# Optimization experiments

Measured on AMD Instinct MI355X. Metric: run time of the kernel, lower is better.

## Reference

```python
import jax, jax.numpy as jnp
import numpy as np

EPS = 1e-5

def layernorm(x, gamma, beta):
    # torch.var default is unbiased (ddof=1) - faithful to source
    m = jnp.mean(x, axis=-1, keepdims=True)
    d = x.shape[-1]
    var = jnp.sum((x - m) ** 2, axis=-1, keepdims=True) / (d - 1)
    return gamma * (x - m) / jnp.sqrt(var + EPS) + beta

def setup_inputs() -> dict:
    key = jax.random.key(0)
    B, S, D, H = 8, 1024, 768, 12
    hd = D // H
    ks = jax.random.split(key, 20)
    s_in = 1.0 / np.sqrt(D)
    s_ff = 1.0 / np.sqrt(4 * D)
    return {
        "x":  jax.random.normal(ks[0], (B, S, D), jnp.float32),
        "Wq": jax.random.uniform(ks[1], (H, D, hd), jnp.float32, -s_in, s_in),
        "bq": jax.random.uniform(ks[2], (H, hd), jnp.float32, -s_in, s_in),
        "Wk": jax.random.uniform(ks[3], (H, D, hd), jnp.float32, -s_in, s_in),
        "bk": jax.random.uniform(ks[4], (H, hd), jnp.float32, -s_in, s_in),
        "Wv": jax.random.uniform(ks[5], (H, D, hd), jnp.float32, -s_in, s_in),
        "bv": jax.random.uniform(ks[6], (H, hd), jnp.float32, -s_in, s_in),
        "Wo": jax.random.uniform(ks[7], (D, D), jnp.float32, -s_in, s_in),
        "bo": jax.random.uniform(ks[8], (D,), jnp.float32, -s_in, s_in),
        "W1": jax.random.uniform(ks[9], (D, 4 * D), jnp.float32, -s_in, s_in),
        "b1": jax.random.uniform(ks[10], (4 * D,), jnp.float32, -s_in, s_in),
        "W2": jax.random.uniform(ks[11], (4 * D, D), jnp.float32, -s_ff, s_ff),
        "b2": jax.random.uniform(ks[12], (D,), jnp.float32, -s_ff, s_ff),
        "g1": jnp.ones((D,), jnp.float32),
        "be1": jnp.zeros((D,), jnp.float32),
        "g2": jnp.ones((D,), jnp.float32),
        "be2": jnp.zeros((D,), jnp.float32),
    }

def reference(x, Wq, bq, Wk, bk, Wv, bv, Wo, bo, W1, b1, W2, b2, g1, be1, g2, be2):
    # x = ln1(x); x = x + mha(x); x = ln2(x); out = x + ffwd(x)
    x = layernorm(x, g1, be1)
    hd = Wq.shape[-1]
    q = jnp.einsum('bsd,hdk->bhsk', x, Wq) + bq[None, :, None, :]
    k = jnp.einsum('bsd,hdk->bhsk', x, Wk) + bk[None, :, None, :]
    v = jnp.einsum('bsd,hdk->bhsk', x, Wv) + bv[None, :, None, :]
    att = jnp.einsum('bhqk,bhsk->bhqs', q, k) * (hd ** -0.5)
    att = jax.nn.softmax(att, axis=-1)
    o = jnp.einsum('bhqs,bhsk->bhqk', att, v)  # [B,H,S,hd]
    B, H, S, _ = o.shape
    o = jnp.transpose(o, (0, 2, 1, 3)).reshape(B, S, H * hd)  # concat heads
    x = x + o @ Wo + bo
    x = layernorm(x, g2, be2)
    h = jax.nn.gelu(x @ W1 + b1, approximate=False)
    out = x + h @ W2 + b2
    return out
```

## Files before the change

### kernel.cpp

```cpp
#include <hip/hip_runtime.h>
#include <stdint.h>

typedef __attribute__((ext_vector_type(8))) short bf16x8;
typedef __attribute__((ext_vector_type(4))) float f32x4;

#define GPTR(p) ((const __attribute__((address_space(1))) void*)(p))
#define LPTR(p) ((__attribute__((address_space(3))) void*)(p))

__device__ __forceinline__ float b2f(unsigned short u) {
  union { unsigned int i; float f; } v; v.i = ((unsigned int)u) << 16; return v.f;
}
__device__ __forceinline__ unsigned short f2b(float f) {
  union { float f; unsigned int i; } v; v.f = f;
  unsigned int i = v.i;
  return (unsigned short)((i + 0x7FFFu + ((i >> 16) & 1u)) >> 16);
}

__global__ __launch_bounds__(256) void ln_kernel(const unsigned short* __restrict__ xin,
                                                 const float* __restrict__ g,
                                                 const float* __restrict__ be,
                                                 unsigned short* __restrict__ y) {
  const int D = 768;
  int row = blockIdx.x;
  int t = threadIdx.x;
  float v[3];
  float s = 0.f, s2 = 0.f;
#pragma unroll
  for (int i = 0; i < 3; ++i) {
    int c = t + i * 256;
    float f = b2f(xin[(size_t)row * D + c]);
    v[i] = f; s += f; s2 += f * f;
  }
#pragma unroll
  for (int d = 32; d > 0; d >>= 1) { s += __shfl_down(s, d); s2 += __shfl_down(s2, d); }
  __shared__ float red[8];
  int w = t >> 6;
  if ((t & 63) == 0) { red[w] = s; red[4 + w] = s2; }
  __syncthreads();
  s = red[0] + red[1] + red[2] + red[3];
  s2 = red[4] + red[5] + red[6] + red[7];
  float mean = s * (1.0f / 768.0f);
  float var = (s2 - 768.0f * mean * mean) * (1.0f / 767.0f);
  float rstd = rsqrtf(var + 1e-5f);
  unsigned short* yr = y + (size_t)row * D;
#pragma unroll
  for (int i = 0; i < 3; ++i) {
    int c = t + i * 256;
    yr[c] = f2b((v[i] - mean) * rstd * g[c] + be[c]);
  }
}

__global__ __launch_bounds__(256) void prep_kernel(const float* __restrict__ Wq,
                                                   const float* __restrict__ Wk,
                                                   const float* __restrict__ Wv,
                                                   const float* __restrict__ Wo,
                                                   const float* __restrict__ W1,
                                                   const float* __restrict__ W2,
                                                   const float* __restrict__ x,
                                                   const float* __restrict__ g1,
                                                   const float* __restrict__ be1,
                                                   unsigned short* __restrict__ Wqkvt,
                                                   unsigned short* __restrict__ Wot,
                                                   unsigned short* __restrict__ W1t,
                                                   unsigned short* __restrict__ W2t,
                                                   unsigned short* __restrict__ y) {
  int bid = blockIdx.x;
  int t = threadIdx.x;
  if (bid < 6912) {
    __shared__ float tile[32][33];
    const float* in; unsigned short* out; int R, C, c0, r0;
    if (bid < 1728) {
      int seg = bid / 576, r = bid % 576;
      int z = r / 48, t2 = r % 48, bx = t2 & 1, by = t2 >> 1;
      in = (seg == 0 ? Wq : seg == 1 ? Wk : Wv) + (size_t)z * 768 * 64;
      out = Wqkvt + (size_t)seg * 768 * 768 + (size_t)z * 64 * 768;
      R = 768; C = 64; c0 = bx * 32; r0 = by * 32;
    } else if (bid < 2304) {
      int r = bid - 1728, bx = r % 24, by = r / 24;
      in = Wo; out = Wot; R = 768; C = 768; c0 = bx * 32; r0 = by * 32;
    } else if (bid < 4608) {
      int r = bid - 2304, bx = r % 96, by = r / 96;
      in = W1; out = W1t; R = 768; C = 3072; c0 = bx * 32; r0 = by * 32;
    } else {
      int r = bid - 4608, bx = r % 24, by = r / 24;
      in = W2; out = W2t; R = 3072; C = 768; c0 = bx * 32; r0 = by * 32;
    }
    int tc = t & 31, tr = t >> 5;
#pragma unroll
    for (int i = 0; i < 4; ++i) {
      int r = tr + i * 8;
      tile[r][tc] = in[(size_t)(r0 + r) * C + c0 + tc];
    }
    __syncthreads();
#pragma unroll
    for (int i = 0; i < 4; ++i) {
      int r = tr + i * 8;
      out[(size_t)(c0 + r) * R + r0 + tc] = f2b(tile[tc][r]);
    }
  } else {
    const int D = 768;
    int row = bid - 6912;
    float v[3];
    float s = 0.f, s2 = 0.f;
#pragma unroll
    for (int i = 0; i < 3; ++i) {
      int c = t + i * 256;
      float f = x[(size_t)row * D + c];
      v[i] = f; s += f; s2 += f * f;
    }
#pragma unroll
    for (int d = 32; d > 0; d >>= 1) { s += __shfl_down(s, d); s2 += __shfl_down(s2, d); }
    __shared__ float red[8];
    int w = t >> 6;
    if ((t & 63) == 0) { red[w] = s; red[4 + w] = s2; }
    __syncthreads();
    s = red[0] + red[1] + red[2] + red[3];
    s2 = red[4] + red[5] + red[6] + red[7];
    float mean = s * (1.0f / 768.0f);
    float var = (s2 - 768.0f * mean * mean) * (1.0f / 767.0f);
    float rstd = rsqrtf(var + 1e-5f);
    unsigned short* yr = y + (size_t)row * D;
#pragma unroll
    for (int i = 0; i < 3; ++i) {
      int c = t + i * 256;
      yr[c] = f2b((v[i] - mean) * rstd * g1[c] + be1[c]);
    }
  }
}

template <int EPI>
__global__ __launch_bounds__(256) void gemm_bt(const unsigned short* __restrict__ A,
                                               const unsigned short* __restrict__ Bt,
                                               int M, int N, int K,
                                               const float* __restrict__ bias0,
                                               const float* __restrict__ bias1,
                                               const float* __restrict__ bias2,
                                               const unsigned short* __restrict__ res,
                                               unsigned short* __restrict__ out0,
                                               unsigned short* __restrict__ out1,
                                               unsigned short* __restrict__ out2,
                                               float* __restrict__ outf) {
  __shared__ unsigned short As[2][128 * 32];
  __shared__ unsigned short Bs[2][128 * 32];
  int t = threadIdx.x;
  int n0 = blockIdx.x * 128, m0 = blockIdx.y * 128;
  int lane = t & 63, w = t >> 6;
  int lr = lane & 15, quad = lane >> 4;
  int wm = (w >> 1) * 64, wn = (w & 1) * 64;
  int rowInWave = lane >> 2;
  int colq = (lane & 3) * 8;
  f32x4 zero4 = {0.f, 0.f, 0.f, 0.f};
  f32x4 acc[4][4];
#pragma unroll
  for (int i = 0; i < 4; ++i)
#pragma unroll
    for (int j = 0; j < 4; ++j) acc[i][j] = zero4;
  for (int k0 = 0; k0 < K; k0 += 64) {
    __syncthreads();
#pragma unroll
    for (int s = 0; s < 2; ++s) {
#pragma unroll
      for (int rnd = 0; rnd < 2; ++rnd) {
        int rbase = rnd * 64 + w * 16;
        int row = rbase + rowInWave;
        __builtin_amdgcn_global_load_lds(GPTR(A + (size_t)(m0 + row) * K + k0 + s * 32 + colq),
                                         LPTR(&As[s][rbase * 32]), 16, 0, 0);
        __builtin_amdgcn_global_load_lds(GPTR(Bt + (size_t)(n0 + row) * K + k0 + s * 32 + colq),
                                         LPTR(&Bs[s][rbase * 32]), 16, 0, 0);
      }
    }
    __syncthreads();
#pragma unroll
    for (int s = 0; s < 2; ++s) {
      bf16x8 af[4];
#pragma unroll
      for (int i = 0; i < 4; ++i)
        af[i] = *(const bf16x8*)(&As[s][(wm + i * 16 + lr) * 32 + quad * 8]);
#pragma unroll
      for (int j = 0; j < 4; ++j) {
        bf16x8 bfr = *(const bf16x8*)(&Bs[s][(wn + j * 16 + lr) * 32 + quad * 8]);
#pragma unroll
        for (int i = 0; i < 4; ++i)
          acc[i][j] = __builtin_amdgcn_mfma_f32_16x16x32_bf16(af[i], bfr, acc[i][j], 0, 0, 0);
      }
    }
  }
#pragma unroll
  for (int i = 0; i < 4; ++i) {
#pragma unroll
    for (int j = 0; j < 4; ++j) {
#pragma unroll
      for (int r = 0; r < 4; ++r) {
        int rg = m0 + wm + i * 16 + quad * 4 + r;
        int cg = n0 + wn + j * 16 + lr;
        float val = acc[i][j][r];
        if (EPI == 1) {
          int b = rg >> 10, sx = rg & 1023;
          if (cg < 768) {
            int h = cg >> 6, kk = cg & 63;
            out0[(((size_t)(b * 12 + h) << 10) + sx) * 64 + kk] = f2b(val + bias0[cg]);
          } else if (cg < 1536) {
            int cc = cg - 768, h = cc >> 6, kk = cc & 63;
            out1[(((size_t)(b * 12 + h) << 10) + sx) * 64 + kk] = f2b(val + bias1[cc]);
          } else {
            int cc = cg - 1536, h = cc >> 6, kk = cc & 63;
            out2[((size_t)(b * 12 + h) << 16) + ((size_t)kk << 10) + sx] = f2b(val + bias2[cc]);
          }
        } else if (EPI == 2) {
          val += bias0[cg] + b2f(res[(size_t)rg * N + cg]);
          out0[(size_t)rg * N + cg] = f2b(val);
        } else if (EPI == 3) {
          float xg = val + bias0[cg];
          val = 0.5f * xg * (1.0f + erff(xg * 0.70710678118654752f));
          out0[(size_t)rg * N + cg] = f2b(val);
        } else if (EPI == 4) {
          outf[(size_t)rg * N + cg] = val + bias0[cg] + b2f(res[(size_t)rg * N + cg]);
        }
      }
    }
  }
}

__global__ __launch_bounds__(256) void attn_kernel(const unsigned short* __restrict__ q,
                                                   const unsigned short* __restrict__ k,
                                                   const unsigned short* __restrict__ vt,
                                                   unsigned short* __restrict__ out) {
  __shared__ unsigned short Ks[64 * 72];
  __shared__ unsigned short Vs[64 * 72];
  __shared__ unsigned short Ps[4][32 * 72];
  int bh = blockIdx.y;
  int q0 = blockIdx.x * 128;
  int t = threadIdx.x, lane = t & 63, w = t >> 6;
  int lr = lane & 15, quad = lane >> 4;
  const unsigned short* qb = q + (size_t)bh * 1024 * 64;
  const unsigned short* kb = k + (size_t)bh * 1024 * 64;
  const unsigned short* vb = vt + (size_t)bh * 64 * 1024;
  bf16x8 aq[2][2];
#pragma unroll
  for (int i = 0; i < 2; ++i)
#pragma unroll
    for (int ks = 0; ks < 2; ++ks)
      aq[i][ks] = *(const bf16x8*)(qb + (size_t)(q0 + w * 32 + i * 16 + lr) * 64 + ks * 32 + quad * 8);
  f32x4 zero4 = {0.f, 0.f, 0.f, 0.f};
  f32x4 oacc[2][4];
  float l_part[2][4];
#pragma unroll
  for (int i = 0; i < 2; ++i)
#pragma unroll
    for (int j = 0; j < 4; ++j) oacc[i][j] = zero4;
#pragma unroll
  for (int i = 0; i < 2; ++i)
#pragma unroll
    for (int r = 0; r < 4; ++r) l_part[i][r] = 0.f;
  int srow = t >> 3, spart = t & 7;
  unsigned short* ps = &Ps[w][0];
  for (int st = 0; st < 16; ++st) {
    int s0 = st * 64;
    __syncthreads();
#pragma unroll
    for (int rnd = 0; rnd < 2; ++rnd) {
      int rr = rnd * 32 + srow;
      *(uint4*)(&Ks[rr * 72 + spart * 8]) = *(const uint4*)(kb + (size_t)(s0 + rr) * 64 + spart * 8);
      *(uint4*)(&Vs[rr * 72 + spart * 8]) = *(const uint4*)(vb + (size_t)rr * 1024 + s0 + spart * 8);
    }
    __syncthreads();
#pragma unroll
    for (int i = 0; i < 2; ++i) {
#pragma unroll
      for (int j = 0; j < 4; ++j) {
        bf16x8 bk0 = *(const bf16x8*)(&Ks[(j * 16 + lr) * 72 + quad * 8]);
        bf16x8 bk1 = *(const bf16x8*)(&Ks[(j * 16 + lr) * 72 + 32 + quad * 8]);
        f32x4 z = zero4;
        z = __builtin_amdgcn_mfma_f32_16x16x32_bf16(aq[i][0], bk0, z, 0, 0, 0);
        z = __builtin_amdgcn_mfma_f32_16x16x32_bf16(aq[i][1], bk1, z, 0, 0, 0);
#pragma unroll
        for (int r = 0; r < 4; ++r) {
          float p = __expf(z[r] * 0.125f);
          l_part[i][r] += p;
          ps[(i * 16 + quad * 4 + r) * 72 + j * 16 + lr] = f2b(p);
        }
      }
    }
    __syncthreads();
#pragma unroll
    for (int i = 0; i < 2; ++i) {
#pragma unroll
      for (int ks = 0; ks < 2; ++ks) {
        bf16x8 ap = *(const bf16x8*)(&ps[(i * 16 + lr) * 72 + ks * 32 + quad * 8]);
#pragma unroll
        for (int j = 0; j < 4; ++j) {
          bf16x8 bv = *(const bf16x8*)(&Vs[(j * 16 + lr) * 72 + ks * 32 + quad * 8]);
          oacc[i][j] = __builtin_amdgcn_mfma_f32_16x16x32_bf16(ap, bv, oacc[i][j], 0, 0, 0);
        }
      }
    }
  }
  int b = bh / 12, h = bh % 12;
#pragma unroll
  for (int i = 0; i < 2; ++i) {
#pragma unroll
    for (int r = 0; r < 4; ++r) {
      float l = l_part[i][r];
#pragma unroll
      for (int d = 1; d < 16; d <<= 1) l += __shfl_xor(l, d);
      float inv = 1.0f / l;
      int sx = q0 + w * 32 + i * 16 + quad * 4 + r;
      size_t base = ((size_t)(b * 1024 + sx)) * 768 + h * 64;
#pragma unroll
      for (int j = 0; j < 4; ++j)
        out[base + j * 16 + lr] = f2b(oacc[i][j][r] * inv);
    }
  }
}

extern "C" void kernel_launch(void* const* d_in, const int* in_sizes, int n_in,
                              void* d_out, int out_size, void* d_ws, size_t ws_size,
                              hipStream_t stream) {
  const float* x  = (const float*)d_in[0];
  const float* Wq = (const float*)d_in[1];
  const float* bq = (const float*)d_in[2];
  const float* Wk = (const float*)d_in[3];
  const float* bk = (const float*)d_in[4];
  const float* Wv = (const float*)d_in[5];
  const float* bv = (const float*)d_in[6];
  const float* Wo = (const float*)d_in[7];
  const float* bo = (const float*)d_in[8];
  const float* W1 = (const float*)d_in[9];
  const float* b1 = (const float*)d_in[10];
  const float* W2 = (const float*)d_in[11];
  const float* b2 = (const float*)d_in[12];
  const float* g1 = (const float*)d_in[13];
  const float* be1= (const float*)d_in[14];
  const float* g2 = (const float*)d_in[15];
  const float* be2= (const float*)d_in[16];
  float* outf = (float*)d_out;

  const size_t SLOT = (size_t)8192 * 768;
  unsigned short* ws = (unsigned short*)d_ws;
  unsigned short* Wqkvt = ws;
  unsigned short* Wot   = Wqkvt + (size_t)2304 * 768;
  unsigned short* W1t   = Wot   + (size_t)768 * 768;
  unsigned short* W2t   = W1t   + (size_t)3072 * 768;
  unsigned short* s0    = W2t   + (size_t)768 * 3072;
  unsigned short* s1    = s0 + SLOT;
  unsigned short* s2    = s1 + SLOT;
  unsigned short* s3    = s2 + SLOT;
  unsigned short* s4    = s3 + SLOT;

  unsigned short* qbuf = s0;
  unsigned short* kbuf = s1;
  unsigned short* y    = s2;
  unsigned short* x2   = s3;
  unsigned short* ao   = s4;
  unsigned short* y2   = s4;
  unsigned short* hb   = s0;
  unsigned short* vtb  = (unsigned short*)d_out;

  prep_kernel<<<6912 + 8192, 256, 0, stream>>>(Wq, Wk, Wv, Wo, W1, W2, x, g1, be1,
                                               Wqkvt, Wot, W1t, W2t, y);

  gemm_bt<1><<<dim3(18, 64), 256, 0, stream>>>(y, Wqkvt, 8192, 2304, 768,
                                               bq, bk, bv, nullptr, qbuf, kbuf, vtb, nullptr);
  attn_kernel<<<dim3(8, 96), 256, 0, stream>>>(qbuf, kbuf, vtb, ao);
  gemm_bt<2><<<dim3(6, 64), 256, 0, stream>>>(ao, Wot, 8192, 768, 768,
                                              bo, nullptr, nullptr, y, x2, nullptr, nullptr, nullptr);
  ln_kernel<<<8192, 256, 0, stream>>>(x2, g2, be2, y2);
  gemm_bt<3><<<dim3(24, 64), 256, 0, stream>>>(y2, W1t, 8192, 3072, 768,
                                               b1, nullptr, nullptr, nullptr, hb, nullptr, nullptr, nullptr);
  gemm_bt<4><<<dim3(6, 64), 256, 0, stream>>>(hb, W2t, 8192, 768, 3072,
                                              b2, nullptr, nullptr, y2, nullptr, nullptr, nullptr, outf);
}
```

Before: 443.6 us.

## Give each wave private double-buffered LDS tiles and drop block barriers

The GEMM main loop is restructured so that each wave loads its own 64-row strips of A and B into a private, double-buffered LDS region with global_load_lds. The next K-slice is prefetched while the current one is consumed, and explicit vmcnt waits replace the two __syncthreads per iteration. The aim is to remove block-wide barrier stalls and overlap loads with MFMA work. In exchange, waves that share the same rows now load them separately, so global/L2 traffic rises, LDS use grows to 64KB per block (which may lower occupancy), and the K step shrinks to 32.

```diff
diff --git a/kernel.cpp b/kernel.cpp
--- a/kernel.cpp
+++ b/kernel.cpp
@@ -140,51 +140,58 @@
                                                unsigned short* __restrict__ out1,
                                                unsigned short* __restrict__ out2,
                                                float* __restrict__ outf) {
-  __shared__ unsigned short As[2][128 * 32];
-  __shared__ unsigned short Bs[2][128 * 32];
+  __shared__ unsigned short L[4][2][2][64 * 32];
   int t = threadIdx.x;
   int n0 = blockIdx.x * 128, m0 = blockIdx.y * 128;
   int lane = t & 63, w = t >> 6;
   int lr = lane & 15, quad = lane >> 4;
   int wm = (w >> 1) * 64, wn = (w & 1) * 64;
-  int rowInWave = lane >> 2;
-  int colq = (lane & 3) * 8;
+  int drow = lane >> 2;
+  int dcol = (lane & 3) * 8;
+  const unsigned short* Ab = A + (size_t)(m0 + wm) * K;
+  const unsigned short* Bb = Bt + (size_t)(n0 + wn) * K;
   f32x4 zero4 = {0.f, 0.f, 0.f, 0.f};
   f32x4 acc[4][4];
 #pragma unroll
   for (int i = 0; i < 4; ++i)
 #pragma unroll
     for (int j = 0; j < 4; ++j) acc[i][j] = zero4;
-  for (int k0 = 0; k0 < K; k0 += 64) {
-    __syncthreads();
-#pragma unroll
-    for (int s = 0; s < 2; ++s) {
-#pragma unroll
-      for (int rnd = 0; rnd < 2; ++rnd) {
-        int rbase = rnd * 64 + w * 16;
-        int row = rbase + rowInWave;
-        __builtin_amdgcn_global_load_lds(GPTR(A + (size_t)(m0 + row) * K + k0 + s * 32 + colq),
-                                         LPTR(&As[s][rbase * 32]), 16, 0, 0);
-        __builtin_amdgcn_global_load_lds(GPTR(Bt + (size_t)(n0 + row) * K + k0 + s * 32 + colq),
-                                         LPTR(&Bs[s][rbase * 32]), 16, 0, 0);
-      }
-    }
-    __syncthreads();
-#pragma unroll
-    for (int s = 0; s < 2; ++s) {
-      bf16x8 af[4];
+
+  const int niter = K >> 5;
+#pragma unroll
+  for (int g = 0; g < 4; ++g) {
+    __builtin_amdgcn_global_load_lds(GPTR(Ab + (size_t)(g * 16 + drow) * K + dcol),
+                                     LPTR(&L[w][0][0][g * 512]), 16, 0, 0);
+    __builtin_amdgcn_global_load_lds(GPTR(Bb + (size_t)(g * 16 + drow) * K + dcol),
+                                     LPTR(&L[w][0][1][g * 512]), 16, 0, 0);
+  }
+  for (int it = 0; it < niter; ++it) {
+    int cur = it & 1, nxt = cur ^ 1;
+    int kn = (it + 1 < niter ? it + 1 : it) << 5;
+#pragma unroll
+    for (int g = 0; g < 4; ++g) {
+      __builtin_amdgcn_global_load_lds(GPTR(Ab + (size_t)(g * 16 + drow) * K + kn + dcol),
+                                       LPTR(&L[w][nxt][0][g * 512]), 16, 0, 0);
+      __builtin_amdgcn_global_load_lds(GPTR(Bb + (size_t)(g * 16 + drow) * K + kn + dcol),
+                                       LPTR(&L[w][nxt][1][g * 512]), 16, 0, 0);
+    }
+    asm volatile("s_waitcnt vmcnt(8)" ::: "memory");
+    const unsigned short* as_ = &L[w][cur][0][0];
+    const unsigned short* bs_ = &L[w][cur][1][0];
+    bf16x8 af[4], bfr[4];
+#pragma unroll
+    for (int i = 0; i < 4; ++i)
+      af[i] = *(const bf16x8*)(&as_[(i * 16 + lr) * 32 + quad * 8]);
+#pragma unroll
+    for (int j = 0; j < 4; ++j)
+      bfr[j] = *(const bf16x8*)(&bs_[(j * 16 + lr) * 32 + quad * 8]);
+#pragma unroll
+    for (int j = 0; j < 4; ++j)
 #pragma unroll
       for (int i = 0; i < 4; ++i)
-        af[i] = *(const bf16x8*)(&As[s][(wm + i * 16 + lr) * 32 + quad * 8]);
-#pragma unroll
-      for (int j = 0; j < 4; ++j) {
-        bf16x8 bfr = *(const bf16x8*)(&Bs[s][(wn + j * 16 + lr) * 32 + quad * 8]);
-#pragma unroll
-        for (int i = 0; i < 4; ++i)
-          acc[i][j] = __builtin_amdgcn_mfma_f32_16x16x32_bf16(af[i], bfr, acc[i][j], 0, 0, 0);
-      }
-    }
-  }
+        acc[i][j] = __builtin_amdgcn_mfma_f32_16x16x32_bf16(af[i], bfr[j], acc[i][j], 0, 0, 0);
+  }
+  asm volatile("s_waitcnt vmcnt(0)" ::: "memory");
 #pragma unroll
   for (int i = 0; i < 4; ++i) {
 #pragma unroll
```

Result: slower. 497.4 us (+12.1%).

## Load GEMM A fragments directly from global and double-buffer B in LDS

Applied to the files above, without the earlier changes.

The GEMM no longer stages the A tile in shared memory: each wave reads its A MFMA fragments straight from global memory into registers. B is still staged in LDS, now double-buffered, with the next 32-wide K slice prefetched while the current one is consumed. This leaves one barrier per 32-wide K step instead of two per 64-wide step and halves the LDS footprint. In exchange, A global-load latency is exposed with no prefetch, the two waves that share the same rows load the same A data twice, and barriers happen more often.

```diff
diff --git a/kernel.cpp b/kernel.cpp
--- a/kernel.cpp
+++ b/kernel.cpp
@@ -140,7 +140,6 @@
                                                unsigned short* __restrict__ out1,
                                                unsigned short* __restrict__ out2,
                                                float* __restrict__ outf) {
-  __shared__ unsigned short As[2][128 * 32];
   __shared__ unsigned short Bs[2][128 * 32];
   int t = threadIdx.x;
   int n0 = blockIdx.x * 128, m0 = blockIdx.y * 128;
@@ -155,35 +154,44 @@
   for (int i = 0; i < 4; ++i)
 #pragma unroll
     for (int j = 0; j < 4; ++j) acc[i][j] = zero4;
-  for (int k0 = 0; k0 < K; k0 += 64) {
-    __syncthreads();
-#pragma unroll
-    for (int s = 0; s < 2; ++s) {
-#pragma unroll
-      for (int rnd = 0; rnd < 2; ++rnd) {
-        int rbase = rnd * 64 + w * 16;
-        int row = rbase + rowInWave;
-        __builtin_amdgcn_global_load_lds(GPTR(A + (size_t)(m0 + row) * K + k0 + s * 32 + colq),
-                                         LPTR(&As[s][rbase * 32]), 16, 0, 0);
-        __builtin_amdgcn_global_load_lds(GPTR(Bt + (size_t)(n0 + row) * K + k0 + s * 32 + colq),
-                                         LPTR(&Bs[s][rbase * 32]), 16, 0, 0);
-      }
-    }
-    __syncthreads();
-#pragma unroll
-    for (int s = 0; s < 2; ++s) {
-      bf16x8 af[4];
+
+  const unsigned short* arow[4];
+#pragma unroll
+  for (int i = 0; i < 4; ++i)
+    arow[i] = A + (size_t)(m0 + wm + i * 16 + lr) * K + quad * 8;
+
+  const int niter = K >> 5;
+#pragma unroll
+  for (int rnd = 0; rnd < 2; ++rnd) {
+    int rbase = rnd * 64 + w * 16;
+    __builtin_amdgcn_global_load_lds(GPTR(Bt + (size_t)(n0 + rbase + rowInWave) * K + colq),
+                                     LPTR(&Bs[0][rbase * 32]), 16, 0, 0);
+  }
+  for (int it = 0; it < niter; ++it) {
+    __syncthreads();
+    int cur = it & 1, nxt = cur ^ 1;
+    int k0 = it << 5;
+    int kn = (it + 1 < niter ? it + 1 : it) << 5;
+#pragma unroll
+    for (int rnd = 0; rnd < 2; ++rnd) {
+      int rbase = rnd * 64 + w * 16;
+      __builtin_amdgcn_global_load_lds(GPTR(Bt + (size_t)(n0 + rbase + rowInWave) * K + kn + colq),
+                                       LPTR(&Bs[nxt][rbase * 32]), 16, 0, 0);
+    }
+    bf16x8 af[4];
+#pragma unroll
+    for (int i = 0; i < 4; ++i)
+      af[i] = *(const bf16x8*)(arow[i] + k0);
+    const unsigned short* bs_ = &Bs[cur][0];
+    bf16x8 bfr[4];
+#pragma unroll
+    for (int j = 0; j < 4; ++j)
+      bfr[j] = *(const bf16x8*)(&bs_[(wn + j * 16 + lr) * 32 + quad * 8]);
+#pragma unroll
+    for (int j = 0; j < 4; ++j)
 #pragma unroll
       for (int i = 0; i < 4; ++i)
-        af[i] = *(const bf16x8*)(&As[s][(wm + i * 16 + lr) * 32 + quad * 8]);
-#pragma unroll
-      for (int j = 0; j < 4; ++j) {
-        bf16x8 bfr = *(const bf16x8*)(&Bs[s][(wn + j * 16 + lr) * 32 + quad * 8]);
-#pragma unroll
-        for (int i = 0; i < 4; ++i)
-          acc[i][j] = __builtin_amdgcn_mfma_f32_16x16x32_bf16(af[i], bfr, acc[i][j], 0, 0, 0);
-      }
-    }
+        acc[i][j] = __builtin_amdgcn_mfma_f32_16x16x32_bf16(af[i], bfr[j], acc[i][j], 0, 0, 0);
   }
 #pragma unroll
   for (int i = 0; i < 4; ++i) {
```

Measured after the change: 539.5 us. +21.6%, slower.
